# Performance work log

Hardware: AMD Instinct MI355X
Metric: run time of the kernel (lower is better)

## Reference

```python
import jax, jax.numpy as jnp
import numpy as np

DECAY = 0.99
LR = 0.01

def setup_inputs() -> dict:
    key = jax.random.key(0)
    ks = jax.random.split(key, 6)
    B, S, D, M = 4, 4096, 1024, 128
    sD = 1.0 / np.sqrt(D)
    sM = 1.0 / np.sqrt(M)
    return {
        "x": jax.random.normal(ks[0], (B, S, D), dtype=jnp.float32),
        "Wk": jax.random.uniform(ks[1], (M, D), jnp.float32, -sD, sD),
        "bk": jnp.zeros((M,), jnp.float32),
        "Wv": jax.random.uniform(ks[2], (M, D), jnp.float32, -sD, sD),
        "bv": jnp.zeros((M,), jnp.float32),
        "Wq": jax.random.uniform(ks[3], (M, D), jnp.float32, -sD, sD),
        "bq": jnp.zeros((M,), jnp.float32),
        "Wo": jax.random.uniform(ks[4], (D, M), jnp.float32, -sM, sM),
        "bo": jnp.zeros((D,), jnp.float32),
    }

def reference(x, Wk, bk, Wv, bv, Wq, bq, Wo, bo):
    B, S, D = x.shape
    M = Wk.shape[0]
    # Precompute all projections in one batched GEMM each: [B,S,M]
    k = jnp.einsum('bsd,md->bsm', x, Wk) + bk
    v = jnp.einsum('bsd,md->bsm', x, Wv) + bv
    q = jnp.einsum('bsd,md->bsm', x, Wq) + bq

    def step(state, kvq):
        k_t, v_t, q_t = kvq  # each [B, M]
        # readout uses the PRE-update state, matching the torch loop order
        out_t = jnp.einsum('bij,bj->bi', state, q_t)          # [B, M]
        state = DECAY * state + LR * jnp.einsum('bi,bj->bij', v_t, k_t)
        return state, out_t

    state0 = jnp.zeros((B, M, M), x.dtype)
    # scan over time: move seq axis to front -> [S, B, M]
    xs = (jnp.swapaxes(k, 0, 1), jnp.swapaxes(v, 0, 1), jnp.swapaxes(q, 0, 1))
    state, outs = jax.lax.scan(step, state0, xs)
    outs = jnp.swapaxes(outs, 0, 1)                            # [B, S, M]
    y = jnp.einsum('bsm,dm->bsd', outs, Wo) + bo               # [B, S, D]
    return (y, state)
```

## Files before the change

### kernel.cpp

```cpp
#include <hip/hip_runtime.h>
#include <math.h>

namespace {
constexpr int kB = 4;
constexpr int kS = 4096;
constexpr int kD = 1024;
constexpr int kM = 128;
constexpr int kC = 64;
constexpr int kNC = kS / kC;
constexpr int kNCG = kB * kNC;
constexpr int kRS = kB * kS;
constexpr float kLR = 0.01f;
constexpr float kLog2d = -0.0144995696f;
}

typedef __bf16 bf16x8 __attribute__((ext_vector_type(8)));
typedef float  f32x4  __attribute__((ext_vector_type(4)));
typedef unsigned short u16;
typedef unsigned int   u32;

__device__ __forceinline__ u16 f2bf(float f) {
  u32 x = __float_as_uint(f);
  u32 r = (x + 0x7fffu + ((x >> 16) & 1u)) >> 16;
  return (u16)r;
}

__device__ __forceinline__ float bf2f(u16 h) {
  return __uint_as_float(((u32)h) << 16);
}

__device__ __forceinline__ void gl_lds16(const void* g, void* l) {
  __builtin_amdgcn_global_load_lds(
      (const __attribute__((address_space(1))) void*)g,
      (__attribute__((address_space(3))) void*)l, 16, 0, 0);
}

__device__ __forceinline__ f32x4 mf(bf16x8 a, bf16x8 b, f32x4 c) {
  return __builtin_amdgcn_mfma_f32_16x16x32_bf16(a, b, c, 0, 0, 0);
}

__device__ __forceinline__ ushort4 pack4(float4 a) {
  ushort4 o;
  o.x = f2bf(a.x); o.y = f2bf(a.y); o.z = f2bf(a.z); o.w = f2bf(a.w);
  return o;
}

__device__ __forceinline__ int fo64x128(int r, int c) {
  return ((r >> 4) * 4 + (c >> 5)) * 1024 + ((c >> 3) & 3) * 256 + (r & 15) * 16 + (c & 7) * 2;
}
__device__ __forceinline__ int fo128x64(int r, int c) {
  return ((r >> 4) * 2 + (c >> 5)) * 1024 + ((c >> 3) & 3) * 256 + (r & 15) * 16 + (c & 7) * 2;
}
__device__ __forceinline__ int fo64x64(int r, int c) {
  return ((r >> 4) * 2 + (c >> 5)) * 1024 + ((c >> 3) & 3) * 256 + (r & 15) * 16 + (c & 7) * 2;
}

__global__ __launch_bounds__(256)
void cast_w_kernel(const float* __restrict__ Wk, const float* __restrict__ Wv,
                   const float* __restrict__ Wq, const float* __restrict__ Wo,
                   u16* __restrict__ Wkvqf, u16* __restrict__ Wohf)
{
  int i = (blockIdx.x * 256 + threadIdx.x) * 4;
  if (i < 393216) {
    const float* src = (i < 131072) ? Wk + i
                     : (i < 262144) ? Wv + (i - 131072) : Wq + (i - 262144);
    float4 v = *(const float4*)src;
    const int n = i >> 10, c = i & 1023;
    const int s = n >> 7, p = (n >> 4) & 7, fr = n & 15;
    const int t = c >> 6, kh = (c >> 5) & 1, qd = (c >> 3) & 3, e = c & 7;
    u16* dst = Wkvqf + ((size_t)((s * 8 + p) * 32 + t * 2 + kh) * 512
                        + qd * 128 + fr * 8 + e);
    *(ushort4*)dst = pack4(v);
  } else {
    const int widx = i - 393216;
    float4 v = *(const float4*)(Wo + widx);
    const int d = widx >> 7, m = widx & 127;
    u16* dst = Wohf + ((size_t)((d >> 4) * 4 + (m >> 5)) * 512
                       + ((m >> 3) & 3) * 128 + (d & 15) * 8 + (m & 7));
    *(ushort4*)dst = pack4(v);
  }
}

__global__ __launch_bounds__(256, 3)
void proj_gemm(const float* __restrict__ x, const u16* __restrict__ Wkvqf,
               const float* __restrict__ bk, const float* __restrict__ bv,
               const float* __restrict__ bq,
               u16* __restrict__ Qg, u16* __restrict__ Kg,
               u16* __restrict__ VTg, u16* __restrict__ KwTg)
{
  __shared__ __align__(16) u16 L[24576];
  const int cg = blockIdx.x, s = blockIdx.y;
  const int R0 = cg * 64;
  const int tid = threadIdx.x, w = tid >> 6, lane = tid & 63;
  const int fr = lane & 15, qd = lane >> 4;
  const int wr = w >> 1, wc = w & 1;

  constexpr int A0 = 0, A1o = 8192, B0 = 16384, B1o = 32768;

  const int xr = tid >> 2, s4 = tid & 3;
  const float* xp = x + (size_t)(R0 + xr) * kD + s4 * 4;
  int aoffq[4];
#pragma unroll
  for (int q = 0; q < 4; ++q)
    aoffq[q] = ((xr >> 4) * 2 + (q >> 1)) * 1024 + (((s4 >> 1) + 2 * q) & 3) * 256
             + (xr & 15) * 16 + (s4 & 1) * 8;

  const u16* wbase = Wkvqf + (size_t)s * 131072 + lane * 8;

  f32x4 acc[2][4] = {};
  float4 xv[4];

  {
#pragma unroll
    for (int g = 0; g < 4; ++g) {
      const int pn = 4 * w + g, p = pn >> 1, kh = pn & 1;
      gl_lds16(wbase + (size_t)(p * 32 + kh) * 512, &L[(B0 + pn * 1024) >> 1]);
    }
    float4 x0[4];
#pragma unroll
    for (int q = 0; q < 4; ++q) x0[q] = *(const float4*)(xp + q * 16);
#pragma unroll
    for (int q = 0; q < 4; ++q) *(ushort4*)&L[(A0 + aoffq[q]) >> 1] = pack4(x0[q]);
#pragma unroll
    for (int q = 0; q < 4; ++q) xv[q] = *(const float4*)(xp + 64 + q * 16);
  }
  __syncthreads();

#pragma unroll 2
  for (int i = 0; i < 16; ++i) {
    const int Ac = (i & 1) ? A1o : A0, Bc = (i & 1) ? B1o : B0;
    const int An = (i & 1) ? A0 : A1o, Bn = (i & 1) ? B0 : B1o;
    if (i < 15) {
      const int t1 = i + 1;
#pragma unroll
      for (int g = 0; g < 4; ++g) {
        const int pn = 4 * w + g, p = pn >> 1, kh = pn & 1;
        gl_lds16(wbase + (size_t)(p * 32 + t1 * 2 + kh) * 512, &L[(Bn + pn * 1024) >> 1]);
      }
#pragma unroll
      for (int q = 0; q < 4; ++q) *(ushort4*)&L[(An + aoffq[q]) >> 1] = pack4(xv[q]);
      if (i < 14) {
#pragma unroll
        for (int q = 0; q < 4; ++q) xv[q] = *(const float4*)(xp + (i + 2) * 64 + q * 16);
      }
    }
    bf16x8 af[2][2], bfr[2][4];
#pragma unroll
    for (int kh = 0; kh < 2; ++kh) {
#pragma unroll
      for (int mi = 0; mi < 2; ++mi)
        af[kh][mi] = *(const bf16x8*)&L[(Ac + ((wr * 2 + mi) * 2 + kh) * 1024 + qd * 256 + fr * 16) >> 1];
#pragma unroll
      for (int ng = 0; ng < 4; ++ng)
        bfr[kh][ng] = *(const bf16x8*)&L[(Bc + ((wc * 4 + ng) * 2 + kh) * 1024 + qd * 256 + fr * 16) >> 1];
    }
#pragma unroll
    for (int kh = 0; kh < 2; ++kh)
#pragma unroll
      for (int mi = 0; mi < 2; ++mi)
#pragma unroll
        for (int ng = 0; ng < 4; ++ng)
          acc[mi][ng] = mf(af[kh][mi], bfr[kh][ng], acc[mi][ng]);
    __syncthreads();
  }

  const float* bp = (s == 0) ? bk : (s == 1) ? bv : bq;
  float bias[4];
#pragma unroll
  for (int ng = 0; ng < 4; ++ng) bias[ng] = bp[wc * 64 + ng * 16 + fr];
  const size_t cb = (size_t)cg * 8192;

  if (s == 0) {
    float dp[2][4];
#pragma unroll
    for (int mi = 0; mi < 2; ++mi)
#pragma unroll
      for (int r = 0; r < 4; ++r)
        dp[mi][r] = kLR * exp2f((float)(63 - (wr * 32 + mi * 16 + qd * 4 + r)) * kLog2d);
#pragma unroll
    for (int mi = 0; mi < 2; ++mi)
#pragma unroll
      for (int ng = 0; ng < 4; ++ng)
#pragma unroll
        for (int r = 0; r < 4; ++r) {
          const int t = wr * 32 + mi * 16 + qd * 4 + r, n = wc * 64 + ng * 16 + fr;
          const float v = acc[mi][ng][r] + bias[ng];
          Kg[cb + (fo64x128(t, n) >> 1)] = f2bf(v);
          KwTg[cb + (fo128x64(n, t) >> 1)] = f2bf(v * dp[mi][r]);
        }
  } else if (s == 1) {
#pragma unroll
    for (int mi = 0; mi < 2; ++mi)
#pragma unroll
      for (int ng = 0; ng < 4; ++ng)
#pragma unroll
        for (int r = 0; r < 4; ++r) {
          const int t = wr * 32 + mi * 16 + qd * 4 + r, n = wc * 64 + ng * 16 + fr;
          VTg[cb + (fo128x64(n, t) >> 1)] = f2bf(acc[mi][ng][r] + bias[ng]);
        }
  } else {
#pragma unroll
    for (int mi = 0; mi < 2; ++mi)
#pragma unroll
      for (int ng = 0; ng < 4; ++ng)
#pragma unroll
        for (int r = 0; r < 4; ++r) {
          const int t = wr * 32 + mi * 16 + qd * 4 + r, n = wc * 64 + ng * 16 + fr;
          Qg[cb + (fo64x128(t, n) >> 1)] = f2bf(acc[mi][ng][r] + bias[ng]);
        }
  }
}

__global__ __launch_bounds__(256, 2)
void intra_kernel(const u16* __restrict__ Qg, const u16* __restrict__ Kg,
                  const u16* __restrict__ VTg, const u16* __restrict__ KwTg,
                  u16* __restrict__ O1g, float* __restrict__ SU)
{
  __shared__ __align__(16) u16 L[28672];
  const int cg = blockIdx.x, ih = blockIdx.y;
  const int tid = threadIdx.x, w = tid >> 6, lane = tid & 63;
  const int fr = lane & 15, qd = lane >> 4;
  const size_t cb = (size_t)cg * 8192;

#pragma unroll
  for (int g = 0; g < 4; ++g) {
    const int pn = 4 * w + g;
    gl_lds16(Qg + cb + pn * 512 + lane * 8, &L[(0 + pn * 1024) >> 1]);
    gl_lds16(Kg + cb + pn * 512 + lane * 8, &L[(16384 + pn * 1024) >> 1]);
    gl_lds16(KwTg + cb + pn * 512 + lane * 8, &L[(40960 + pn * 1024) >> 1]);
  }
#pragma unroll
  for (int g = 0; g < 2; ++g) {
    const int p2 = 2 * w + g;
    gl_lds16(VTg + cb + ih * 4096 + p2 * 512 + lane * 8, &L[(32768 + p2 * 1024) >> 1]);
  }
  __syncthreads();

  f32x4 p[4] = {};
#pragma unroll
  for (int kc = 0; kc < 4; ++kc) {
    bf16x8 aq = *(const bf16x8*)&L[(0 + (w * 4 + kc) * 1024 + qd * 256 + fr * 16) >> 1];
#pragma unroll
    for (int ug = 0; ug < 4; ++ug) {
      bf16x8 bkf = *(const bf16x8*)&L[(16384 + (ug * 4 + kc) * 1024 + qd * 256 + fr * 16) >> 1];
      p[ug] = mf(aq, bkf, p[ug]);
    }
  }
  __syncthreads();

#pragma unroll
  for (int ug = 0; ug < 4; ++ug)
#pragma unroll
    for (int r = 0; r < 4; ++r) {
      const int t = w * 16 + qd * 4 + r, u = ug * 16 + fr;
      float av = 0.f;
      if (u < t) av = kLR * exp2f((float)(t - 1 - u) * kLog2d) * p[ug][r];
      L[(16384 + fo64x64(t, u)) >> 1] = f2bf(av);
    }
  __syncthreads();

  f32x4 o1[4] = {}, uu[8] = {};
#pragma unroll
  for (int kc = 0; kc < 2; ++kc) {
    bf16x8 aA = *(const bf16x8*)&L[(16384 + (w * 2 + kc) * 1024 + qd * 256 + fr * 16) >> 1];
    bf16x8 aV = *(const bf16x8*)&L[(32768 + (w * 2 + kc) * 1024 + qd * 256 + fr * 16) >> 1];
#pragma unroll
    for (int ni = 0; ni < 4; ++ni) {
      bf16x8 bV = *(const bf16x8*)&L[(32768 + (ni * 2 + kc) * 1024 + qd * 256 + fr * 16) >> 1];
      o1[ni] = mf(aA, bV, o1[ni]);
    }
#pragma unroll
    for (int jf = 0; jf < 8; ++jf) {
      bf16x8 bK = *(const bf16x8*)&L[(40960 + (jf * 2 + kc) * 1024 + qd * 256 + fr * 16) >> 1];
      uu[jf] = mf(aV, bK, uu[jf]);
    }
  }

#pragma unroll
  for (int ni = 0; ni < 4; ++ni)
#pragma unroll
    for (int r = 0; r < 4; ++r) {
      const int t = w * 16 + qd * 4 + r, i2 = (ih * 4 + ni) * 16 + fr;
      O1g[cb + (fo64x128(t, i2) >> 1)] = f2bf(o1[ni][r]);
    }
  float* SUc = SU + (size_t)cg * 16384;
#pragma unroll
  for (int jf = 0; jf < 8; ++jf)
#pragma unroll
    for (int r = 0; r < 4; ++r) {
      const int i2 = ih * 64 + w * 16 + qd * 4 + r, j = jf * 16 + fr;
      SUc[i2 * kM + j] = uu[jf][r];
    }
}

__global__ __launch_bounds__(128)
void scan_kernel(const float* __restrict__ SU, u16* __restrict__ Sb16,
                 float* __restrict__ state_out)
{
  const int e = blockIdx.x * 128 + threadIdx.x;
  const int b = e >> 14, ij = e & 16383;
  const float* base = SU + (size_t)b * kNC * 16384 + ij;
  u16* sb = Sb16 + (size_t)b * kNC * 16384 + ij;
  const float dC = exp2f((float)kC * kLog2d);
  float prev = 0.f;
#pragma unroll 16
  for (int c2 = 0; c2 < kNC; ++c2) {
    const float u = base[(size_t)c2 * 16384];
    sb[(size_t)c2 * 16384] = f2bf(prev);
    prev = fmaf(dC, prev, u);
  }
  state_out[e] = prev;
}

__global__ __launch_bounds__(256, 2)
void fco(const u16* __restrict__ Qg, const u16* __restrict__ Sb16,
         const u16* __restrict__ O1g, const u16* __restrict__ Wohf,
         const float* __restrict__ bo, float* __restrict__ y)
{
  __shared__ __align__(16) u16 L[24576];
  const int cg = blockIdx.x, th = blockIdx.y;
  const int tid = threadIdx.x, w = tid >> 6, lane = tid & 63;
  const int fr = lane & 15, qd = lane >> 4;
  const size_t cb = (size_t)cg * 8192;
  const u16* Sbc = Sb16 + (size_t)cg * 16384;

#pragma unroll
  for (int g = 0; g < 2; ++g) {
    const int p = 2 * w + g;
    gl_lds16(Qg + cb + (th * 8 + p) * 512 + lane * 8, &L[(0 + p * 1024) >> 1]);
    gl_lds16(O1g + cb + (th * 8 + p) * 512 + lane * 8, &L[(40960 + p * 1024) >> 1]);
  }
#pragma unroll
  for (int g = 0; g < 8; ++g) {
    const int pn = 8 * w + g, ig = pn >> 2, kc = pn & 3;
    gl_lds16(Sbc + (size_t)(ig * 16 + fr) * kM + kc * 32 + qd * 8,
             &L[(8192 + pn * 1024) >> 1]);
  }
  __syncthreads();

  const int tf2 = w >> 1, ihl = w & 1;
  f32x4 o2[4] = {};
#pragma unroll
  for (int kc = 0; kc < 4; ++kc) {
    bf16x8 aq = *(const bf16x8*)&L[(0 + (tf2 * 4 + kc) * 1024 + qd * 256 + fr * 16) >> 1];
#pragma unroll
    for (int ni = 0; ni < 4; ++ni) {
      bf16x8 bS = *(const bf16x8*)&L[(8192 + ((ihl * 4 + ni) * 4 + kc) * 1024 + qd * 256 + fr * 16) >> 1];
      o2[ni] = mf(aq, bS, o2[ni]);
    }
  }
  __syncthreads();

#pragma unroll
  for (int ni = 0; ni < 4; ++ni)
#pragma unroll
    for (int r = 0; r < 4; ++r) {
      const int tl = tf2 * 16 + qd * 4 + r;
      const int tg = th * 32 + tl;
      const int i2 = (ihl * 4 + ni) * 16 + fr;
      const float o1v = bf2f(L[(40960 + fo64x128(tl, i2)) >> 1]);
      L[(0 + fo64x128(tl, i2)) >> 1] =
          f2bf(fmaf(exp2f((float)tg * kLog2d), o2[ni][r], o1v));
    }
  __syncthreads();

  const int R0 = cg * 64 + th * 32;
#pragma unroll 1
  for (int h = 0; h < 2; ++h) {
    const int n0 = w * 256 + h * 128;
    f32x4 fy[2][8] = {};
#pragma unroll
    for (int kc = 0; kc < 4; ++kc) {
      bf16x8 ao[2], bw[8];
#pragma unroll
      for (int mi = 0; mi < 2; ++mi)
        ao[mi] = *(const bf16x8*)&L[((mi * 4 + kc) * 1024 + qd * 256 + fr * 16) >> 1];
#pragma unroll
      for (int nj = 0; nj < 8; ++nj)
        bw[nj] = *(const bf16x8*)&Wohf[((size_t)(w * 16 + h * 8 + nj) * 4 + kc) * 512 + lane * 8];
#pragma unroll
      for (int mi = 0; mi < 2; ++mi)
#pragma unroll
        for (int nj = 0; nj < 8; ++nj)
          fy[mi][nj] = mf(ao[mi], bw[nj], fy[mi][nj]);
    }
#pragma unroll
    for (int nj = 0; nj < 8; ++nj) {
      const int d = n0 + nj * 16 + fr;
      const float bb = bo[d];
#pragma unroll
      for (int mi = 0; mi < 2; ++mi)
#pragma unroll
        for (int r = 0; r < 4; ++r)
          y[(size_t)(R0 + mi * 16 + qd * 4 + r) * kD + d] = fy[mi][nj][r] + bb;
    }
  }
}

extern "C" void kernel_launch(void* const* d_in, const int* in_sizes, int n_in,
                              void* d_out, int out_size, void* d_ws, size_t ws_size,
                              hipStream_t stream) {
  const float* x  = (const float*)d_in[0];
  const float* Wk = (const float*)d_in[1];
  const float* bk = (const float*)d_in[2];
  const float* Wv = (const float*)d_in[3];
  const float* bv = (const float*)d_in[4];
  const float* Wq = (const float*)d_in[5];
  const float* bq = (const float*)d_in[6];
  const float* Wo = (const float*)d_in[7];
  const float* bo = (const float*)d_in[8];

  char* wsp = (char*)d_ws;
  u16* Wkvqf = (u16*)wsp; wsp += (size_t)384 * 1024 * 2;
  u16* Wohf  = (u16*)wsp; wsp += (size_t)1024 * 128 * 2;
  u16* Qg    = (u16*)wsp; wsp += (size_t)kNCG * 8192 * 2;
  u16* Kg    = (u16*)wsp; wsp += (size_t)kNCG * 8192 * 2;
  u16* VTg   = (u16*)wsp;
  u16* KwTg  = VTg + (size_t)kNCG * 8192;
  u16* Sb16  = VTg;
  wsp += (size_t)kNCG * 16384 * 2;
  u16* O1g   = (u16*)wsp; wsp += (size_t)kNCG * 8192 * 2;
  float* SU  = (float*)wsp; wsp += (size_t)kNCG * 16384 * 4;

  float* y = (float*)d_out;
  float* state_out = y + (size_t)kRS * kD;

  cast_w_kernel<<<dim3(512), dim3(256), 0, stream>>>(Wk, Wv, Wq, Wo, Wkvqf, Wohf);
  proj_gemm<<<dim3(kNCG, 3), dim3(256), 0, stream>>>(x, Wkvqf, bk, bv, bq, Qg, Kg, VTg, KwTg);
  intra_kernel<<<dim3(kNCG, 2), dim3(256), 0, stream>>>(Qg, Kg, VTg, KwTg, O1g, SU);
  scan_kernel<<<dim3(kB * 16384 / 128), dim3(128), 0, stream>>>(SU, Sb16, state_out);
  fco<<<dim3(kNCG, 2), dim3(256), 0, stream>>>(Qg, Sb16, O1g, Wohf, bo, y);
}
```

Before: 174.1 us.

## Load Q and O1 fragments into registers to shrink LDS and raise occupancy

In both the intra-chunk and output kernels, the Q (and O1) MFMA fragments are now read straight from global memory into registers instead of staged through LDS. This cuts the LDS footprint of each kernel to 40 KB and lifts the launch bound from 2 to 4 blocks per CU. O1 now goes to global in a fragment-native packed layout with vectorized stores, which also removes one LDS round-trip and a barrier in fco. The trade-off is more register pressure under the tighter launch bound and uncoalesced-per-fragment global reads.

```diff
diff --git a/kernel.cpp b/kernel.cpp
--- a/kernel.cpp
+++ b/kernel.cpp
@@ -211,23 +211,27 @@
   }
 }
 
-__global__ __launch_bounds__(256, 2)
+__global__ __launch_bounds__(256, 4)
 void intra_kernel(const u16* __restrict__ Qg, const u16* __restrict__ Kg,
                   const u16* __restrict__ VTg, const u16* __restrict__ KwTg,
                   u16* __restrict__ O1g, float* __restrict__ SU)
 {
-  __shared__ __align__(16) u16 L[28672];
+  __shared__ __align__(16) u16 L[20480];
   const int cg = blockIdx.x, ih = blockIdx.y;
   const int tid = threadIdx.x, w = tid >> 6, lane = tid & 63;
   const int fr = lane & 15, qd = lane >> 4;
   const size_t cb = (size_t)cg * 8192;
 
+  bf16x8 aq[4];
+#pragma unroll
+  for (int kc = 0; kc < 4; ++kc)
+    aq[kc] = *(const bf16x8*)(Qg + cb + (w * 4 + kc) * 512 + qd * 128 + fr * 8);
+
 #pragma unroll
   for (int g = 0; g < 4; ++g) {
     const int pn = 4 * w + g;
-    gl_lds16(Qg + cb + pn * 512 + lane * 8, &L[(0 + pn * 1024) >> 1]);
-    gl_lds16(Kg + cb + pn * 512 + lane * 8, &L[(16384 + pn * 1024) >> 1]);
-    gl_lds16(KwTg + cb + pn * 512 + lane * 8, &L[(40960 + pn * 1024) >> 1]);
+    gl_lds16(KwTg + cb + pn * 512 + lane * 8, &L[(0 + pn * 1024) >> 1]);
+    gl_lds16(Kg  + cb + pn * 512 + lane * 8, &L[(16384 + pn * 1024) >> 1]);
   }
 #pragma unroll
   for (int g = 0; g < 2; ++g) {
@@ -239,11 +243,10 @@
   f32x4 p[4] = {};
 #pragma unroll
   for (int kc = 0; kc < 4; ++kc) {
-    bf16x8 aq = *(const bf16x8*)&L[(0 + (w * 4 + kc) * 1024 + qd * 256 + fr * 16) >> 1];
 #pragma unroll
     for (int ug = 0; ug < 4; ++ug) {
       bf16x8 bkf = *(const bf16x8*)&L[(16384 + (ug * 4 + kc) * 1024 + qd * 256 + fr * 16) >> 1];
-      p[ug] = mf(aq, bkf, p[ug]);
+      p[ug] = mf(aq[kc], bkf, p[ug]);
     }
   }
   __syncthreads();
@@ -271,18 +274,18 @@
     }
 #pragma unroll
     for (int jf = 0; jf < 8; ++jf) {
-      bf16x8 bK = *(const bf16x8*)&L[(40960 + (jf * 2 + kc) * 1024 + qd * 256 + fr * 16) >> 1];
+      bf16x8 bK = *(const bf16x8*)&L[(0 + (jf * 2 + kc) * 1024 + qd * 256 + fr * 16) >> 1];
       uu[jf] = mf(aV, bK, uu[jf]);
     }
   }
 
 #pragma unroll
-  for (int ni = 0; ni < 4; ++ni)
-#pragma unroll
-    for (int r = 0; r < 4; ++r) {
-      const int t = w * 16 + qd * 4 + r, i2 = (ih * 4 + ni) * 16 + fr;
-      O1g[cb + (fo64x128(t, i2) >> 1)] = f2bf(o1[ni][r]);
-    }
+  for (int ni = 0; ni < 4; ++ni) {
+    ushort4 o;
+    o.x = f2bf(o1[ni][0]); o.y = f2bf(o1[ni][1]);
+    o.z = f2bf(o1[ni][2]); o.w = f2bf(o1[ni][3]);
+    *(ushort4*)(O1g + cb + (size_t)((w * 8 + ih * 4 + ni) * 64 + lane) * 4) = o;
+  }
   float* SUc = SU + (size_t)cg * 16384;
 #pragma unroll
   for (int jf = 0; jf < 8; ++jf)
@@ -312,56 +315,64 @@
   state_out[e] = prev;
 }
 
-__global__ __launch_bounds__(256, 2)
+__global__ __launch_bounds__(256, 4)
 void fco(const u16* __restrict__ Qg, const u16* __restrict__ Sb16,
          const u16* __restrict__ O1g, const u16* __restrict__ Wohf,
          const float* __restrict__ bo, float* __restrict__ y)
 {
-  __shared__ __align__(16) u16 L[24576];
+  __shared__ __align__(16) u16 L[20480];
   const int cg = blockIdx.x, th = blockIdx.y;
   const int tid = threadIdx.x, w = tid >> 6, lane = tid & 63;
   const int fr = lane & 15, qd = lane >> 4;
   const size_t cb = (size_t)cg * 8192;
   const u16* Sbc = Sb16 + (size_t)cg * 16384;
 
-#pragma unroll
-  for (int g = 0; g < 2; ++g) {
-    const int p = 2 * w + g;
-    gl_lds16(Qg + cb + (th * 8 + p) * 512 + lane * 8, &L[(0 + p * 1024) >> 1]);
-    gl_lds16(O1g + cb + (th * 8 + p) * 512 + lane * 8, &L[(40960 + p * 1024) >> 1]);
-  }
+  const int tf2 = w >> 1, ihl = w & 1;
+  const int tfg = th * 2 + tf2;
+
+  bf16x8 aq[4];
+#pragma unroll
+  for (int kc = 0; kc < 4; ++kc)
+    aq[kc] = *(const bf16x8*)(Qg + cb + (tfg * 4 + kc) * 512 + qd * 128 + fr * 8);
+  ushort4 o1h[4];
+#pragma unroll
+  for (int ni = 0; ni < 4; ++ni)
+    o1h[ni] = *(const ushort4*)(O1g + cb +
+        (size_t)((tfg * 8 + ihl * 4 + ni) * 64 + lane) * 4);
+
 #pragma unroll
   for (int g = 0; g < 8; ++g) {
     const int pn = 8 * w + g, ig = pn >> 2, kc = pn & 3;
     gl_lds16(Sbc + (size_t)(ig * 16 + fr) * kM + kc * 32 + qd * 8,
-             &L[(8192 + pn * 1024) >> 1]);
-  }
-  __syncthreads();
-
-  const int tf2 = w >> 1, ihl = w & 1;
+             &L[(0 + pn * 1024) >> 1]);
+  }
+  __syncthreads();
+
   f32x4 o2[4] = {};
 #pragma unroll
   for (int kc = 0; kc < 4; ++kc) {
-    bf16x8 aq = *(const bf16x8*)&L[(0 + (tf2 * 4 + kc) * 1024 + qd * 256 + fr * 16) >> 1];
 #pragma unroll
     for (int ni = 0; ni < 4; ++ni) {
-      bf16x8 bS = *(const bf16x8*)&L[(8192 + ((ihl * 4 + ni) * 4 + kc) * 1024 + qd * 256 + fr * 16) >> 1];
-      o2[ni] = mf(aq, bS, o2[ni]);
-    }
-  }
-  __syncthreads();
-
-#pragma unroll
-  for (int ni = 0; ni < 4; ++ni)
+      bf16x8 bS = *(const bf16x8*)&L[(0 + ((ihl * 4 + ni) * 4 + kc) * 1024 + qd * 256 + fr * 16) >> 1];
+      o2[ni] = mf(aq[kc], bS, o2[ni]);
+    }
+  }
+
+  float dt[4];
+#pragma unroll
+  for (int r = 0; r < 4; ++r)
+    dt[r] = exp2f((float)(th * 32 + tf2 * 16 + qd * 4 + r) * kLog2d);
+#pragma unroll
+  for (int ni = 0; ni < 4; ++ni) {
+    const u16 oh[4] = {o1h[ni].x, o1h[ni].y, o1h[ni].z, o1h[ni].w};
 #pragma unroll
     for (int r = 0; r < 4; ++r) {
       const int tl = tf2 * 16 + qd * 4 + r;
-      const int tg = th * 32 + tl;
       const int i2 = (ihl * 4 + ni) * 16 + fr;
-      const float o1v = bf2f(L[(40960 + fo64x128(tl, i2)) >> 1]);
-      L[(0 + fo64x128(tl, i2)) >> 1] =
-          f2bf(fmaf(exp2f((float)tg * kLog2d), o2[ni][r], o1v));
-    }
+      L[(32768 + fo64x128(tl, i2)) >> 1] =
+          f2bf(fmaf(dt[r], o2[ni][r], bf2f(oh[r])));
+    }
+  }
   __syncthreads();
 
   const int R0 = cg * 64 + th * 32;
@@ -374,7 +385,7 @@
       bf16x8 ao[2], bw[8];
 #pragma unroll
       for (int mi = 0; mi < 2; ++mi)
-        ao[mi] = *(const bf16x8*)&L[((mi * 4 + kc) * 1024 + qd * 256 + fr * 16) >> 1];
+        ao[mi] = *(const bf16x8*)&L[(32768 + (mi * 4 + kc) * 1024 + qd * 256 + fr * 16) >> 1];
 #pragma unroll
       for (int nj = 0; nj < 8; ++nj)
         bw[nj] = *(const bf16x8*)&Wohf[((size_t)(w * 16 + h * 8 + nj) * 4 + kc) * 512 + lane * 8];
```

Result: slower. 182.2 us (+4.6%).

## Load projection weights straight into registers and split warps by output columns

Applied to the files above, without the earlier changes.

The projection GEMM stops staging weight tiles through LDS. Each wave now owns 32 output columns across all 64 rows and loads its weight fragments directly from global memory into registers, double-buffered across K steps. Only x goes through LDS, which shrinks LDS use from 48KB to 16KB, and the barriers become a lighter lgkmcnt wait plus s_barrier. The tradeoff is more register pressure and global weight loads no longer shared across waves, with direct-register global latency partly hidden by the manual unroll.

```diff
diff --git a/kernel.cpp b/kernel.cpp
--- a/kernel.cpp
+++ b/kernel.cpp
@@ -18,6 +18,9 @@
 typedef float  f32x4  __attribute__((ext_vector_type(4)));
 typedef unsigned short u16;
 typedef unsigned int   u32;
+
+#define LBAR() do { asm volatile("s_waitcnt lgkmcnt(0)" ::: "memory"); \
+                    __builtin_amdgcn_s_barrier(); } while (0)
 
 __device__ __forceinline__ u16 f2bf(float f) {
   u32 x = __float_as_uint(f);
@@ -88,14 +91,11 @@
                u16* __restrict__ Qg, u16* __restrict__ Kg,
                u16* __restrict__ VTg, u16* __restrict__ KwTg)
 {
-  __shared__ __align__(16) u16 L[24576];
+  __shared__ __align__(16) u16 L[8192];
   const int cg = blockIdx.x, s = blockIdx.y;
   const int R0 = cg * 64;
   const int tid = threadIdx.x, w = tid >> 6, lane = tid & 63;
   const int fr = lane & 15, qd = lane >> 4;
-  const int wr = w >> 1, wc = w & 1;
-
-  constexpr int A0 = 0, A1o = 8192, B0 = 16384, B1o = 32768;
 
   const int xr = tid >> 2, s4 = tid & 3;
   const float* xp = x + (size_t)(R0 + xr) * kD + s4 * 4;
@@ -107,105 +107,101 @@
 
   const u16* wbase = Wkvqf + (size_t)s * 131072 + lane * 8;
 
-  f32x4 acc[2][4] = {};
+  f32x4 acc[4][2] = {};
+  bf16x8 bA[4], bB[4];
   float4 xv[4];
 
-  {
-#pragma unroll
-    for (int g = 0; g < 4; ++g) {
-      const int pn = 4 * w + g, p = pn >> 1, kh = pn & 1;
-      gl_lds16(wbase + (size_t)(p * 32 + kh) * 512, &L[(B0 + pn * 1024) >> 1]);
-    }
-    float4 x0[4];
-#pragma unroll
-    for (int q = 0; q < 4; ++q) x0[q] = *(const float4*)(xp + q * 16);
-#pragma unroll
-    for (int q = 0; q < 4; ++q) *(ushort4*)&L[(A0 + aoffq[q]) >> 1] = pack4(x0[q]);
-#pragma unroll
-    for (int q = 0; q < 4; ++q) xv[q] = *(const float4*)(xp + 64 + q * 16);
-  }
-  __syncthreads();
-
-#pragma unroll 2
-  for (int i = 0; i < 16; ++i) {
-    const int Ac = (i & 1) ? A1o : A0, Bc = (i & 1) ? B1o : B0;
-    const int An = (i & 1) ? A0 : A1o, Bn = (i & 1) ? B0 : B1o;
-    if (i < 15) {
-      const int t1 = i + 1;
-#pragma unroll
-      for (int g = 0; g < 4; ++g) {
-        const int pn = 4 * w + g, p = pn >> 1, kh = pn & 1;
-        gl_lds16(wbase + (size_t)(p * 32 + t1 * 2 + kh) * 512, &L[(Bn + pn * 1024) >> 1]);
-      }
-#pragma unroll
-      for (int q = 0; q < 4; ++q) *(ushort4*)&L[(An + aoffq[q]) >> 1] = pack4(xv[q]);
-      if (i < 14) {
-#pragma unroll
-        for (int q = 0; q < 4; ++q) xv[q] = *(const float4*)(xp + (i + 2) * 64 + q * 16);
-      }
-    }
-    bf16x8 af[2][2], bfr[2][4];
-#pragma unroll
-    for (int kh = 0; kh < 2; ++kh) {
-#pragma unroll
-      for (int mi = 0; mi < 2; ++mi)
-        af[kh][mi] = *(const bf16x8*)&L[(Ac + ((wr * 2 + mi) * 2 + kh) * 1024 + qd * 256 + fr * 16) >> 1];
-#pragma unroll
-      for (int ng = 0; ng < 4; ++ng)
-        bfr[kh][ng] = *(const bf16x8*)&L[(Bc + ((wc * 4 + ng) * 2 + kh) * 1024 + qd * 256 + fr * 16) >> 1];
-    }
+  auto loadB = [&](int t, bf16x8 (&bs)[4]) {
+#pragma unroll
+    for (int ng = 0; ng < 2; ++ng)
+#pragma unroll
+      for (int kh = 0; kh < 2; ++kh)
+        bs[ng * 2 + kh] = *(const bf16x8*)(wbase +
+            (size_t)((w * 2 + ng) * 32 + t * 2 + kh) * 512);
+  };
+  auto writeA = [&](int Abuf) {
+#pragma unroll
+    for (int q = 0; q < 4; ++q)
+      *(ushort4*)&L[(Abuf + aoffq[q]) >> 1] = pack4(xv[q]);
+  };
+  auto loadX = [&](int t) {
+#pragma unroll
+    for (int q = 0; q < 4; ++q) xv[q] = *(const float4*)(xp + t * 64 + q * 16);
+  };
+  auto compute = [&](int Abuf, bf16x8 (&bs)[4]) {
+    bf16x8 af[2][4];
 #pragma unroll
     for (int kh = 0; kh < 2; ++kh)
 #pragma unroll
-      for (int mi = 0; mi < 2; ++mi)
-#pragma unroll
-        for (int ng = 0; ng < 4; ++ng)
-          acc[mi][ng] = mf(af[kh][mi], bfr[kh][ng], acc[mi][ng]);
-    __syncthreads();
-  }
+      for (int mi = 0; mi < 4; ++mi)
+        af[kh][mi] = *(const bf16x8*)&L[(Abuf + (mi * 2 + kh) * 1024 + qd * 256 + fr * 16) >> 1];
+#pragma unroll
+    for (int kh = 0; kh < 2; ++kh)
+#pragma unroll
+      for (int mi = 0; mi < 4; ++mi)
+#pragma unroll
+        for (int ng = 0; ng < 2; ++ng)
+          acc[mi][ng] = mf(af[kh][mi], bs[ng * 2 + kh], acc[mi][ng]);
+  };
+
+  loadB(0, bA);
+  loadX(0); writeA(0);
+  loadX(1);
+  LBAR();
+
+  for (int it = 0; it < 7; ++it) {
+    const int t = 2 * it;
+    loadB(t + 1, bB); writeA(8192); loadX(t + 2);
+    compute(0, bA);   LBAR();
+    loadB(t + 2, bA); writeA(0);    loadX(t + 3);
+    compute(8192, bB); LBAR();
+  }
+  loadB(15, bB); writeA(8192);
+  compute(0, bA); LBAR();
+  compute(8192, bB);
 
   const float* bp = (s == 0) ? bk : (s == 1) ? bv : bq;
-  float bias[4];
-#pragma unroll
-  for (int ng = 0; ng < 4; ++ng) bias[ng] = bp[wc * 64 + ng * 16 + fr];
+  float bias[2];
+#pragma unroll
+  for (int ng = 0; ng < 2; ++ng) bias[ng] = bp[w * 32 + ng * 16 + fr];
   const size_t cb = (size_t)cg * 8192;
 
   if (s == 0) {
-    float dp[2][4];
-#pragma unroll
-    for (int mi = 0; mi < 2; ++mi)
+    float dp[4][4];
+#pragma unroll
+    for (int mi = 0; mi < 4; ++mi)
 #pragma unroll
       for (int r = 0; r < 4; ++r)
-        dp[mi][r] = kLR * exp2f((float)(63 - (wr * 32 + mi * 16 + qd * 4 + r)) * kLog2d);
-#pragma unroll
-    for (int mi = 0; mi < 2; ++mi)
-#pragma unroll
-      for (int ng = 0; ng < 4; ++ng)
+        dp[mi][r] = kLR * exp2f((float)(63 - (mi * 16 + qd * 4 + r)) * kLog2d);
+#pragma unroll
+    for (int mi = 0; mi < 4; ++mi)
+#pragma unroll
+      for (int ng = 0; ng < 2; ++ng)
 #pragma unroll
         for (int r = 0; r < 4; ++r) {
-          const int t = wr * 32 + mi * 16 + qd * 4 + r, n = wc * 64 + ng * 16 + fr;
+          const int t = mi * 16 + qd * 4 + r, n = w * 32 + ng * 16 + fr;
           const float v = acc[mi][ng][r] + bias[ng];
           Kg[cb + (fo64x128(t, n) >> 1)] = f2bf(v);
           KwTg[cb + (fo128x64(n, t) >> 1)] = f2bf(v * dp[mi][r]);
         }
   } else if (s == 1) {
 #pragma unroll
-    for (int mi = 0; mi < 2; ++mi)
-#pragma unroll
-      for (int ng = 0; ng < 4; ++ng)
+    for (int mi = 0; mi < 4; ++mi)
+#pragma unroll
+      for (int ng = 0; ng < 2; ++ng)
 #pragma unroll
         for (int r = 0; r < 4; ++r) {
-          const int t = wr * 32 + mi * 16 + qd * 4 + r, n = wc * 64 + ng * 16 + fr;
+          const int t = mi * 16 + qd * 4 + r, n = w * 32 + ng * 16 + fr;
           VTg[cb + (fo128x64(n, t) >> 1)] = f2bf(acc[mi][ng][r] + bias[ng]);
         }
   } else {
 #pragma unroll
-    for (int mi = 0; mi < 2; ++mi)
-#pragma unroll
-      for (int ng = 0; ng < 4; ++ng)
+    for (int mi = 0; mi < 4; ++mi)
+#pragma unroll
+      for (int ng = 0; ng < 2; ++ng)
 #pragma unroll
         for (int r = 0; r < 4; ++r) {
-          const int t = wr * 32 + mi * 16 + qd * 4 + r, n = wc * 64 + ng * 16 + fr;
+          const int t = mi * 16 + qd * 4 + r, n = w * 32 + ng * 16 + fr;
           Qg[cb + (fo64x128(t, n) >> 1)] = f2bf(acc[mi][ng][r] + bias[ng]);
         }
   }
```

After: 179.3 us. 3.0% more time.

## Split intra and output kernels into four blocks per chunk for more parallelism

Applied to the files above, without the earlier changes.

The intra-chunk kernel and the fused output kernel now each launch four blocks per chunk instead of two. Each block handles a quarter of the state rows or time rows, and the launch bounds are raised to allow more resident blocks per CU. This aims to fill the GPU better with 256 chunks across 256 CUs and to reduce per-block LDS and registers. The cost is redundant recomputation of the Q·K^T score tile in every intra block, and the full state tile is reloaded four times in fco.

```diff
diff --git a/kernel.cpp b/kernel.cpp
--- a/kernel.cpp
+++ b/kernel.cpp
@@ -53,6 +53,9 @@
 }
 __device__ __forceinline__ int fo64x64(int r, int c) {
   return ((r >> 4) * 2 + (c >> 5)) * 1024 + ((c >> 3) & 3) * 256 + (r & 15) * 16 + (c & 7) * 2;
+}
+__device__ __forceinline__ int fo16x128(int r, int c) {
+  return (c >> 5) * 1024 + ((c >> 3) & 3) * 256 + (r & 15) * 16 + (c & 7) * 2;
 }
 
 __global__ __launch_bounds__(256)
@@ -211,13 +214,13 @@
   }
 }
 
-__global__ __launch_bounds__(256, 2)
+__global__ __launch_bounds__(256, 3)
 void intra_kernel(const u16* __restrict__ Qg, const u16* __restrict__ Kg,
                   const u16* __restrict__ VTg, const u16* __restrict__ KwTg,
                   u16* __restrict__ O1g, float* __restrict__ SU)
 {
-  __shared__ __align__(16) u16 L[28672];
-  const int cg = blockIdx.x, ih = blockIdx.y;
+  __shared__ __align__(16) u16 L[26624];
+  const int cg = blockIdx.x, iq = blockIdx.y;
   const int tid = threadIdx.x, w = tid >> 6, lane = tid & 63;
   const int fr = lane & 15, qd = lane >> 4;
   const size_t cb = (size_t)cg * 8192;
@@ -227,23 +230,23 @@
     const int pn = 4 * w + g;
     gl_lds16(Qg + cb + pn * 512 + lane * 8, &L[(0 + pn * 1024) >> 1]);
     gl_lds16(Kg + cb + pn * 512 + lane * 8, &L[(16384 + pn * 1024) >> 1]);
-    gl_lds16(KwTg + cb + pn * 512 + lane * 8, &L[(40960 + pn * 1024) >> 1]);
-  }
-#pragma unroll
-  for (int g = 0; g < 2; ++g) {
-    const int p2 = 2 * w + g;
-    gl_lds16(VTg + cb + ih * 4096 + p2 * 512 + lane * 8, &L[(32768 + p2 * 1024) >> 1]);
-  }
-  __syncthreads();
-
-  f32x4 p[4] = {};
+    gl_lds16(KwTg + cb + pn * 512 + lane * 8, &L[(32768 + pn * 1024) >> 1]);
+  }
+  {
+    const int p = w;
+    gl_lds16(VTg + cb + ((iq * 2 + (p >> 1)) * 2 + (p & 1)) * 512 + lane * 8,
+             &L[(49152 + p * 1024) >> 1]);
+  }
+  __syncthreads();
+
+  f32x4 p4[4] = {};
 #pragma unroll
   for (int kc = 0; kc < 4; ++kc) {
     bf16x8 aq = *(const bf16x8*)&L[(0 + (w * 4 + kc) * 1024 + qd * 256 + fr * 16) >> 1];
 #pragma unroll
     for (int ug = 0; ug < 4; ++ug) {
       bf16x8 bkf = *(const bf16x8*)&L[(16384 + (ug * 4 + kc) * 1024 + qd * 256 + fr * 16) >> 1];
-      p[ug] = mf(aq, bkf, p[ug]);
+      p4[ug] = mf(aq, bkf, p4[ug]);
     }
   }
   __syncthreads();
@@ -254,43 +257,49 @@
     for (int r = 0; r < 4; ++r) {
       const int t = w * 16 + qd * 4 + r, u = ug * 16 + fr;
       float av = 0.f;
-      if (u < t) av = kLR * exp2f((float)(t - 1 - u) * kLog2d) * p[ug][r];
+      if (u < t) av = kLR * exp2f((float)(t - 1 - u) * kLog2d) * p4[ug][r];
       L[(16384 + fo64x64(t, u)) >> 1] = f2bf(av);
     }
   __syncthreads();
 
-  f32x4 o1[4] = {}, uu[8] = {};
+  f32x4 o1[2] = {}, uu[2][2] = {};
 #pragma unroll
   for (int kc = 0; kc < 2; ++kc) {
     bf16x8 aA = *(const bf16x8*)&L[(16384 + (w * 2 + kc) * 1024 + qd * 256 + fr * 16) >> 1];
-    bf16x8 aV = *(const bf16x8*)&L[(32768 + (w * 2 + kc) * 1024 + qd * 256 + fr * 16) >> 1];
-#pragma unroll
-    for (int ni = 0; ni < 4; ++ni) {
-      bf16x8 bV = *(const bf16x8*)&L[(32768 + (ni * 2 + kc) * 1024 + qd * 256 + fr * 16) >> 1];
-      o1[ni] = mf(aA, bV, o1[ni]);
-    }
-#pragma unroll
-    for (int jf = 0; jf < 8; ++jf) {
-      bf16x8 bK = *(const bf16x8*)&L[(40960 + (jf * 2 + kc) * 1024 + qd * 256 + fr * 16) >> 1];
-      uu[jf] = mf(aV, bK, uu[jf]);
-    }
-  }
-
-#pragma unroll
-  for (int ni = 0; ni < 4; ++ni)
+    bf16x8 aV[2];
+#pragma unroll
+    for (int il = 0; il < 2; ++il)
+      aV[il] = *(const bf16x8*)&L[(49152 + (il * 2 + kc) * 1024 + qd * 256 + fr * 16) >> 1];
+#pragma unroll
+    for (int il = 0; il < 2; ++il)
+      o1[il] = mf(aA, aV[il], o1[il]);
+#pragma unroll
+    for (int jfl = 0; jfl < 2; ++jfl) {
+      bf16x8 bK = *(const bf16x8*)&L[(32768 + ((2 * w + jfl) * 2 + kc) * 1024 + qd * 256 + fr * 16) >> 1];
+#pragma unroll
+      for (int il = 0; il < 2; ++il)
+        uu[il][jfl] = mf(aV[il], bK, uu[il][jfl]);
+    }
+  }
+
+#pragma unroll
+  for (int il = 0; il < 2; ++il)
 #pragma unroll
     for (int r = 0; r < 4; ++r) {
-      const int t = w * 16 + qd * 4 + r, i2 = (ih * 4 + ni) * 16 + fr;
-      O1g[cb + (fo64x128(t, i2) >> 1)] = f2bf(o1[ni][r]);
+      const int t = w * 16 + qd * 4 + r, i2 = iq * 32 + il * 16 + fr;
+      O1g[cb + (fo64x128(t, i2) >> 1)] = f2bf(o1[il][r]);
     }
   float* SUc = SU + (size_t)cg * 16384;
 #pragma unroll
-  for (int jf = 0; jf < 8; ++jf)
-#pragma unroll
-    for (int r = 0; r < 4; ++r) {
-      const int i2 = ih * 64 + w * 16 + qd * 4 + r, j = jf * 16 + fr;
-      SUc[i2 * kM + j] = uu[jf][r];
-    }
+  for (int il = 0; il < 2; ++il)
+#pragma unroll
+    for (int jfl = 0; jfl < 2; ++jfl)
+#pragma unroll
+      for (int r = 0; r < 4; ++r) {
+        const int i2 = iq * 32 + il * 16 + qd * 4 + r;
+        const int j = (2 * w + jfl) * 16 + fr;
+        SUc[i2 * kM + j] = uu[il][jfl][r];
+      }
 }
 
 __global__ __launch_bounds__(128)
@@ -312,87 +321,79 @@
   state_out[e] = prev;
 }
 
-__global__ __launch_bounds__(256, 2)
+__global__ __launch_bounds__(256, 4)
 void fco(const u16* __restrict__ Qg, const u16* __restrict__ Sb16,
          const u16* __restrict__ O1g, const u16* __restrict__ Wohf,
          const float* __restrict__ bo, float* __restrict__ y)
 {
-  __shared__ __align__(16) u16 L[24576];
-  const int cg = blockIdx.x, th = blockIdx.y;
+  __shared__ __align__(16) u16 L[20480];
+  const int cg = blockIdx.x, tq = blockIdx.y;
   const int tid = threadIdx.x, w = tid >> 6, lane = tid & 63;
   const int fr = lane & 15, qd = lane >> 4;
   const size_t cb = (size_t)cg * 8192;
   const u16* Sbc = Sb16 + (size_t)cg * 16384;
 
 #pragma unroll
-  for (int g = 0; g < 2; ++g) {
-    const int p = 2 * w + g;
-    gl_lds16(Qg + cb + (th * 8 + p) * 512 + lane * 8, &L[(0 + p * 1024) >> 1]);
-    gl_lds16(O1g + cb + (th * 8 + p) * 512 + lane * 8, &L[(40960 + p * 1024) >> 1]);
-  }
-#pragma unroll
   for (int g = 0; g < 8; ++g) {
-    const int pn = 8 * w + g, ig = pn >> 2, kc = pn & 3;
-    gl_lds16(Sbc + (size_t)(ig * 16 + fr) * kM + kc * 32 + qd * 8,
-             &L[(8192 + pn * 1024) >> 1]);
-  }
-  __syncthreads();
-
-  const int tf2 = w >> 1, ihl = w & 1;
-  f32x4 o2[4] = {};
+    const int pn = 8 * w + g, ig = pn >> 2, kc2 = pn & 3;
+    gl_lds16(Sbc + (size_t)(ig * 16 + fr) * kM + kc2 * 32 + qd * 8,
+             &L[(0 + pn * 1024) >> 1]);
+  }
+  gl_lds16(Qg + cb + (tq * 4 + w) * 512 + lane * 8, &L[(32768 + w * 1024) >> 1]);
+  gl_lds16(O1g + cb + (tq * 4 + w) * 512 + lane * 8, &L[(36864 + w * 1024) >> 1]);
+  __syncthreads();
+
+  f32x4 o2[2] = {};
 #pragma unroll
   for (int kc = 0; kc < 4; ++kc) {
-    bf16x8 aq = *(const bf16x8*)&L[(0 + (tf2 * 4 + kc) * 1024 + qd * 256 + fr * 16) >> 1];
-#pragma unroll
-    for (int ni = 0; ni < 4; ++ni) {
-      bf16x8 bS = *(const bf16x8*)&L[(8192 + ((ihl * 4 + ni) * 4 + kc) * 1024 + qd * 256 + fr * 16) >> 1];
-      o2[ni] = mf(aq, bS, o2[ni]);
-    }
-  }
-  __syncthreads();
-
-#pragma unroll
-  for (int ni = 0; ni < 4; ++ni)
+    bf16x8 aq = *(const bf16x8*)&L[(32768 + kc * 1024 + qd * 256 + fr * 16) >> 1];
+#pragma unroll
+    for (int il = 0; il < 2; ++il) {
+      bf16x8 bS = *(const bf16x8*)&L[(0 + ((2 * w + il) * 4 + kc) * 1024 + qd * 256 + fr * 16) >> 1];
+      o2[il] = mf(aq, bS, o2[il]);
+    }
+  }
+  __syncthreads();
+
+  float dt[4];
+#pragma unroll
+  for (int r = 0; r < 4; ++r)
+    dt[r] = exp2f((float)(tq * 16 + qd * 4 + r) * kLog2d);
+#pragma unroll
+  for (int il = 0; il < 2; ++il)
 #pragma unroll
     for (int r = 0; r < 4; ++r) {
-      const int tl = tf2 * 16 + qd * 4 + r;
-      const int tg = th * 32 + tl;
-      const int i2 = (ihl * 4 + ni) * 16 + fr;
-      const float o1v = bf2f(L[(40960 + fo64x128(tl, i2)) >> 1]);
-      L[(0 + fo64x128(tl, i2)) >> 1] =
-          f2bf(fmaf(exp2f((float)tg * kLog2d), o2[ni][r], o1v));
-    }
-  __syncthreads();
-
-  const int R0 = cg * 64 + th * 32;
+      const int tl = qd * 4 + r;
+      const int i2 = (2 * w + il) * 16 + fr;
+      const int off = fo16x128(tl, i2);
+      const float o1v = bf2f(L[(36864 + off) >> 1]);
+      L[(32768 + off) >> 1] = f2bf(fmaf(dt[r], o2[il][r], o1v));
+    }
+  __syncthreads();
+
+  const int R0 = cg * 64 + tq * 16;
 #pragma unroll 1
   for (int h = 0; h < 2; ++h) {
     const int n0 = w * 256 + h * 128;
-    f32x4 fy[2][8] = {};
+    f32x4 fy[8] = {};
 #pragma unroll
     for (int kc = 0; kc < 4; ++kc) {
-      bf16x8 ao[2], bw[8];
-#pragma unroll
-      for (int mi = 0; mi < 2; ++mi)
-        ao[mi] = *(const bf16x8*)&L[((mi * 4 + kc) * 1024 + qd * 256 + fr * 16) >> 1];
+      bf16x8 ao = *(const bf16x8*)&L[(32768 + kc * 1024 + qd * 256 + fr * 16) >> 1];
+      bf16x8 bw[8];
 #pragma unroll
       for (int nj = 0; nj < 8; ++nj)
         bw[nj] = *(const bf16x8*)&Wohf[((size_t)(w * 16 + h * 8 + nj) * 4 + kc) * 512 + lane * 8];
 #pragma unroll
-      for (int mi = 0; mi < 2; ++mi)
-#pragma unroll
-        for (int nj = 0; nj < 8; ++nj)
-          fy[mi][nj] = mf(ao[mi], bw[nj], fy[mi][nj]);
+      for (int nj = 0; nj < 8; ++nj)
+        fy[nj] = mf(ao, bw[nj], fy[nj]);
     }
 #pragma unroll
     for (int nj = 0; nj < 8; ++nj) {
       const int d = n0 + nj * 16 + fr;
       const float bb = bo[d];
 #pragma unroll
-      for (int mi = 0; mi < 2; ++mi)
-#pragma unroll
-        for (int r = 0; r < 4; ++r)
-          y[(size_t)(R0 + mi * 16 + qd * 4 + r) * kD + d] = fy[mi][nj][r] + bb;
+      for (int r = 0; r < 4; ++r)
+        y[(size_t)(R0 + qd * 4 + r) * kD + d] = fy[nj][r] + bb;
     }
   }
 }
@@ -427,7 +428,7 @@
 
   cast_w_kernel<<<dim3(512), dim3(256), 0, stream>>>(Wk, Wv, Wq, Wo, Wkvqf, Wohf);
   proj_gemm<<<dim3(kNCG, 3), dim3(256), 0, stream>>>(x, Wkvqf, bk, bv, bq, Qg, Kg, VTg, KwTg);
-  intra_kernel<<<dim3(kNCG, 2), dim3(256), 0, stream>>>(Qg, Kg, VTg, KwTg, O1g, SU);
+  intra_kernel<<<dim3(kNCG, 4), dim3(256), 0, stream>>>(Qg, Kg, VTg, KwTg, O1g, SU);
   scan_kernel<<<dim3(kB * 16384 / 128), dim3(128), 0, stream>>>(SU, Sb16, state_out);
-  fco<<<dim3(kNCG, 2), dim3(256), 0, stream>>>(Qg, Sb16, O1g, Wohf, bo, y);
-}
+  fco<<<dim3(kNCG, 4), dim3(256), 0, stream>>>(Qg, Sb16, O1g, Wohf, bo, y);
+}
```

Result: no change. 177.4 us (+1.9%).
